# Kernel tuning notes

Hardware: AMD Instinct MI355X
Metric: run time of the kernel (lower is better)

## Reference

```python
import jax, jax.numpy as jnp
import numpy as np

VOCAB = 62
HID = 100
NLAYERS = 3
B, T = 512, 1024


def setup_inputs() -> dict:
    key = jax.random.key(0)
    ks = jax.random.split(key, 8)
    s = 1.0 / np.sqrt(HID)  # PyTorch RNN init scale
    input_ids = jax.random.randint(ks[0], (B, T), 0, VOCAB, dtype=jnp.int32)
    emb = jax.random.normal(ks[1], (VOCAB, HID), dtype=jnp.float32)
    W_ih = jax.random.uniform(ks[2], (NLAYERS, HID, HID), jnp.float32, -s, s)
    W_hh = jax.random.uniform(ks[3], (NLAYERS, HID, HID), jnp.float32, -s, s)
    b_ih = jax.random.uniform(ks[4], (NLAYERS, HID), jnp.float32, -s, s)
    b_hh = jax.random.uniform(ks[5], (NLAYERS, HID), jnp.float32, -s, s)
    W_dec = jax.random.uniform(ks[6], (VOCAB, HID), jnp.float32, -s, s)
    b_dec = jax.random.uniform(ks[7], (VOCAB,), jnp.float32, -s, s)
    return {
        "input_ids": input_ids,
        "emb": emb,
        "W_ih": W_ih,
        "W_hh": W_hh,
        "b_ih": b_ih,
        "b_hh": b_hh,
        "W_dec": W_dec,
        "b_dec": b_dec,
    }


def _rnn_forward(x, W_ih, W_hh, b_ih, b_hh):
    # x: [B, T, H]; multi-layer tanh RNN, zero initial hidden (hidden=None path)
    bsz = x.shape[0]
    finals = []
    layer_in = jnp.swapaxes(x, 0, 1)  # time-major [T, B, H]
    for l in range(NLAYERS):
        Wi, Wh = W_ih[l], W_hh[l]
        bi, bh = b_ih[l], b_hh[l]
        # precompute input projection for whole sequence (one big GEMM)
        xin = jnp.einsum("tbh,kh->tbk", layer_in, Wi) + bi + bh

        def step(h, xt):
            h_new = jnp.tanh(xt + h @ Wh.T)
            return h_new, h_new

        h0 = jnp.zeros((bsz, HID), dtype=x.dtype)
        h_final, ys = jax.lax.scan(step, h0, xin)
        finals.append(h_final)
        layer_in = ys
    out = jnp.swapaxes(layer_in, 0, 1)  # [B, T, H]
    hidden = jnp.stack(finals, axis=0)  # [NLAYERS, B, H]
    return out, hidden


def reference(input_ids, emb, W_ih, W_hh, b_ih, b_hh, W_dec, b_dec):
    x = emb[input_ids]  # [B, T, H] embedding lookup
    rnn_out, hidden = _rnn_forward(x, W_ih, W_hh, b_ih, b_hh)
    logits = jnp.einsum("bth,vh->btv", rnn_out, W_dec) + b_dec  # [B, T, VOCAB]
    return logits, hidden
```

## Files before the change

### kernel.cpp

```cpp
#include <hip/hip_runtime.h>

#define BB 512
#define TT 1024
#define HH 100
#define HP 112
#define VV 62
#define BTV (512*1024*62)

#define OFF_EP  52428800
#define OFF_WP  52435000
#define OFF_BS  52491000
#define OFF_WDT 52491200
#define OFF_BDP 52497600

__device__ inline float tanh_fast(float x){
  float ax = fabsf(x);
  float e  = __expf(2.0f*ax);
  float r  = 1.0f - __fdividef(2.0f, e + 1.0f);
  return copysignf(r, x);
}

__global__ void prep_kernel(
    const float* __restrict__ emb, const float* __restrict__ W_ih,
    const float* __restrict__ W_hh,
    const float* __restrict__ b_ih, const float* __restrict__ b_hh,
    const float* __restrict__ W_dec, const float* __restrict__ b_dec,
    float* __restrict__ ws)
{
  int g = blockIdx.x*256 + threadIdx.x;
  if (g < 6200){
    int v = g/100, k = g%100;
    float a = b_ih[k] + b_hh[k];
    const float* er = emb + v*100;
    const float* wr = W_ih + k*100;
    for (int h=0; h<100; h++) a = fmaf(er[h], wr[h], a);
    ws[OFF_EP + v*100 + k] = a;
  } else if (g < 62200){
    int i = g - 6200;
    int u = i/11200, r = i%11200;
    int k = r/112, h = r%112;
    int l = (u+1)>>1;
    const float* src = (u & 1) ? W_ih : W_hh;
    ws[OFF_WP + i] = (h < HH) ? src[l*10000 + k*100 + h] : 0.f;
  } else if (g < 62400){
    int i = g - 62200;
    int l = i/100 + 1, k = i%100;
    ws[OFF_BS + i] = b_ih[l*100+k] + b_hh[l*100+k];
  } else if (g < 68800){
    int i = g - 62400;
    int h = i/64, v = i%64;
    ws[OFF_WDT + i] = (v < VV) ? W_dec[v*100 + h] : 0.f;
  } else if (g < 68864){
    int i = g - 68800;
    ws[OFF_BDP + i] = (i < VV) ? b_dec[i] : 0.f;
  }
}

#define BARRIER() do{ asm volatile("s_waitcnt lgkmcnt(0)" ::: "memory"); \
                      __builtin_amdgcn_s_barrier(); \
                      asm volatile("" ::: "memory"); }while(0)

__global__ __launch_bounds__(512, 2) void fused_rnn(
    const int* __restrict__ ids, const float* __restrict__ ws,
    float* __restrict__ buf, float* __restrict__ hid)
{
  __shared__ float ep_s[6200];
  __shared__ int   ids_s[2][TT];
  __shared__ float hs[2][3][HP];
  __shared__ float zz[2][2][HH];

  const int tid = threadIdx.x;
  const int bA = blockIdx.x;
  const int bB = blockIdx.x + 256;

  int u = tid / 100;
  int L = tid - u*100;
  const bool act = (tid < 500);
  if (!act){ u = 4; L = 99; }
  const int o4 = (L & ~3);
  const int sq = L & 3;
  const bool is_b0 = (L & 1);
  const bool is_b1 = (L & 2);

  float4 w[4][7];
  #pragma unroll
  for (int j=0;j<4;j++){
    const float4* wr = (const float4*)(ws + OFF_WP + u*11200 + (o4+j)*HP + 28*sq);
    #pragma unroll
    for (int i=0;i<7;i++) w[j][i] = wr[i];
  }
  float binit[4] = {0.f,0.f,0.f,0.f};
  if ((u==1 || u==3) && sq==0){
    const float* bsrow = ws + OFF_BS + (u==3 ? 100 : 0);
    #pragma unroll
    for (int j=0;j<4;j++) binit[j] = bsrow[o4+j];
  }

  for (int i=tid;i<6200;i+=512) ep_s[i] = ws[OFF_EP+i];
  for (int i=tid;i<TT;i+=512){
    ids_s[0][i] = ids[(size_t)bA*TT + i];
    ids_s[1][i] = ids[(size_t)bB*TT + i];
  }
  for (int i=tid;i<2*3*HP;i+=512) ((float*)hs)[i] = 0.f;
  __syncthreads();

  const int lin = (u<=1) ? 0 : (u<=3 ? 1 : 2);
  const float* hinA = &hs[0][lin][28*sq];
  const float* hinB = &hs[1][lin][28*sq];

  int idnA = ids_s[0][1], idnB = ids_s[1][1];
  float epxA = ep_s[ids_s[0][0]*HH + L];
  float epxB = ep_s[ids_s[1][0]*HH + L];
  float epxA_n = 0.f, epxB_n = 0.f;

  float* stA = buf + (size_t)bA*HH + L;
  float* stB = buf + (size_t)bB*HH + L;

  auto quad_reduce = [&](float a0,float a1,float a2,float a3)->float{
    float sA = is_b0 ? a0 : a1, kA = is_b0 ? a1 : a0;
    float A  = kA + __shfl_xor(sA, 1);
    float sB = is_b0 ? a2 : a3, kB = is_b0 ? a3 : a2;
    float Bq = kB + __shfl_xor(sB, 1);
    float sC = is_b1 ? A : Bq, kC = is_b1 ? Bq : A;
    return kC + __shfl_xor(sC, 2);
  };

  for (int s=0; s<TT+2; ++s){
    float aA0=binit[0], aA1=binit[1], aA2=binit[2], aA3=binit[3];
    float aB0=binit[0], aB1=binit[1], aB2=binit[2], aB3=binit[3];
    #pragma unroll
    for (int i=0;i<7;i++){
      float4 ha = ((const float4*)hinA)[i];
      float4 hb = ((const float4*)hinB)[i];
      float4 w0=w[0][i], w1=w[1][i], w2=w[2][i], w3=w[3][i];
      aA0=fmaf(ha.x,w0.x,aA0); aA0=fmaf(ha.y,w0.y,aA0); aA0=fmaf(ha.z,w0.z,aA0); aA0=fmaf(ha.w,w0.w,aA0);
      aA1=fmaf(ha.x,w1.x,aA1); aA1=fmaf(ha.y,w1.y,aA1); aA1=fmaf(ha.z,w1.z,aA1); aA1=fmaf(ha.w,w1.w,aA1);
      aA2=fmaf(ha.x,w2.x,aA2); aA2=fmaf(ha.y,w2.y,aA2); aA2=fmaf(ha.z,w2.z,aA2); aA2=fmaf(ha.w,w2.w,aA2);
      aA3=fmaf(ha.x,w3.x,aA3); aA3=fmaf(ha.y,w3.y,aA3); aA3=fmaf(ha.z,w3.z,aA3); aA3=fmaf(ha.w,w3.w,aA3);
      aB0=fmaf(hb.x,w0.x,aB0); aB0=fmaf(hb.y,w0.y,aB0); aB0=fmaf(hb.z,w0.z,aB0); aB0=fmaf(hb.w,w0.w,aB0);
      aB1=fmaf(hb.x,w1.x,aB1); aB1=fmaf(hb.y,w1.y,aB1); aB1=fmaf(hb.z,w1.z,aB1); aB1=fmaf(hb.w,w1.w,aB1);
      aB2=fmaf(hb.x,w2.x,aB2); aB2=fmaf(hb.y,w2.y,aB2); aB2=fmaf(hb.z,w2.z,aB2); aB2=fmaf(hb.w,w2.w,aB2);
      aB3=fmaf(hb.x,w3.x,aB3); aB3=fmaf(hb.y,w3.y,aB3); aB3=fmaf(hb.z,w3.z,aB3); aB3=fmaf(hb.w,w3.w,aB3);
    }
    float zA = quad_reduce(aA0,aA1,aA2,aA3);
    float zB = quad_reduce(aB0,aB1,aB2,aB3);

    if (u==0){
      epxA_n = ep_s[idnA*HH + L];
      epxB_n = ep_s[idnB*HH + L];
      int nid = (s+2 < TT) ? s+2 : TT-1;
      idnA = ids_s[0][nid]; idnB = ids_s[1][nid];
    }
    if (u==2){        zz[0][0][L] = zA; zz[1][0][L] = zB; }
    if (u==4 && act){ zz[0][1][L] = zA; zz[1][1][L] = zB; }
    BARRIER();

    if (u==0 && s < TT){
      float hA = tanh_fast(epxA + zA);
      float hB = tanh_fast(epxB + zB);
      hs[0][0][L] = hA; hs[1][0][L] = hB;
      epxA = epxA_n; epxB = epxB_n;
    }
    if (u==1 && (unsigned)(s-1) < TT){
      hs[0][1][L] = tanh_fast(zA + zz[0][0][L]);
      hs[1][1][L] = tanh_fast(zB + zz[1][0][L]);
    }
    if (u==3 && s >= 2){
      float hA = tanh_fast(zA + zz[0][1][L]);
      float hB = tanh_fast(zB + zz[1][1][L]);
      hs[0][2][L] = hA; hs[1][2][L] = hB;
      *stA = hA; *stB = hB;
      stA += BB*HH; stB += BB*HH;
    }
    BARRIER();
  }
  __syncthreads();

  if (tid < 300){
    int l = tid/100, k = tid - l*100;
    hid[((size_t)l*BB + bA)*HH + k] = hs[0][l][k];
    hid[((size_t)l*BB + bB)*HH + k] = hs[1][l][k];
  }
}

__global__ __launch_bounds__(128) void dec_kernel(
    const float* __restrict__ buf, const float* __restrict__ wdt,
    const float* __restrict__ bdp, float* __restrict__ out)
{
  __shared__ float rt[100*129];
  const int tid = threadIdx.x;
  const int wg  = blockIdx.x;
  const int bb  = wg >> 3;
  const int t0  = (wg & 7) * 128;
  const float4* b4 = (const float4*)buf;

  #pragma unroll
  for (int j=0;j<25;j++){
    int f = j*128 + tid;
    int i = f/25, c = f%25;
    float4 v = b4[((size_t)(t0+i)*BB + bb)*25 + c];
    rt[(4*c+0)*129 + i] = v.x;
    rt[(4*c+1)*129 + i] = v.y;
    rt[(4*c+2)*129 + i] = v.z;
    rt[(4*c+3)*129 + i] = v.w;
  }
  __syncthreads();

  float4 acc[16];
  const float4* bd4 = (const float4*)bdp;
  #pragma unroll
  for (int j=0;j<16;j++) acc[j] = bd4[j];

  for (int h=0; h<HH; h++){
    float rv = rt[h*129 + tid];
    const float4* w4 = (const float4*)(wdt + h*64);
    #pragma unroll
    for (int j=0;j<16;j++){
      float4 w = w4[j];
      acc[j].x = fmaf(rv,w.x,acc[j].x);
      acc[j].y = fmaf(rv,w.y,acc[j].y);
      acc[j].z = fmaf(rv,w.z,acc[j].z);
      acc[j].w = fmaf(rv,w.w,acc[j].w);
    }
  }

  float2* o2 = (float2*)(out + (size_t)(wg*128 + tid)*VV);
  #pragma unroll
  for (int j=0;j<15;j++){
    o2[2*j]   = make_float2(acc[j].x, acc[j].y);
    o2[2*j+1] = make_float2(acc[j].z, acc[j].w);
  }
  o2[30] = make_float2(acc[15].x, acc[15].y);
}

extern "C" void kernel_launch(void* const* d_in, const int* in_sizes, int n_in,
                              void* d_out, int out_size, void* d_ws, size_t ws_size,
                              hipStream_t stream)
{
  const int*   ids   = (const int*)d_in[0];
  const float* emb   = (const float*)d_in[1];
  const float* W_ih  = (const float*)d_in[2];
  const float* W_hh  = (const float*)d_in[3];
  const float* b_ih  = (const float*)d_in[4];
  const float* b_hh  = (const float*)d_in[5];
  const float* W_dec = (const float*)d_in[6];
  const float* b_dec = (const float*)d_in[7];
  float* out = (float*)d_out;
  float* ws  = (float*)d_ws;
  float* buf = ws;
  float* hid = out + BTV;

  prep_kernel<<<269, 256, 0, stream>>>(emb, W_ih, W_hh, b_ih, b_hh, W_dec, b_dec, ws);
  fused_rnn <<<256, 512, 0, stream>>>(ids, ws, buf, hid);
  dec_kernel<<<4096, 128, 0, stream>>>(buf, ws+OFF_WDT, ws+OFF_BDP, out);
}
```

Before: 1.518 ms.

## Restructure fused RNN to one barrier per step with double-buffered hidden state

Reassigns the hidden-state work so each layer's input and recurrent matvecs for one output row are done by the same lane group. This removes the intermediate zz exchange and halves the barriers per timestep, using double-buffered hidden-state tiles in shared memory. It also uses packed v2f FMAs and DPP cross-lane reductions instead of shuffles, writes the intermediate buffer batch-major so the decoder reads contiguous rows, and writes final hidden states inline. In exchange each lane holds 112 weight floats in registers, which adds register pressure under launch_bounds(512,2).

Result: faster. 1.369 ms (-9.8%).

```diff
diff --git a/kernel.cpp b/kernel.cpp
--- a/kernel.cpp
+++ b/kernel.cpp
@@ -3,21 +3,29 @@
 #define BB 512
 #define TT 1024
 #define HH 100
-#define HP 112
 #define VV 62
 #define BTV (512*1024*62)
 
 #define OFF_EP  52428800
-#define OFF_WP  52435000
-#define OFF_BS  52491000
-#define OFF_WDT 52491200
-#define OFF_BDP 52497600
+#define OFF_WU  52435200
+#define OFF_BS  52491200
+#define OFF_WDT 52491400
+#define OFF_BDP 52497800
+
+typedef float v2f __attribute__((ext_vector_type(2)));
 
 __device__ inline float tanh_fast(float x){
   float ax = fabsf(x);
   float e  = __expf(2.0f*ax);
   float r  = 1.0f - __fdividef(2.0f, e + 1.0f);
   return copysignf(r, x);
+}
+
+__device__ inline float dpp_xor1(float x){
+  return __int_as_float(__builtin_amdgcn_update_dpp(0, __float_as_int(x), 0xB1, 0xF, 0xF, true));
+}
+__device__ inline float dpp_xor2(float x){
+  return __int_as_float(__builtin_amdgcn_update_dpp(0, __float_as_int(x), 0x4E, 0xF, 0xF, true));
 }
 
 __global__ void prep_kernel(
@@ -37,11 +45,30 @@
     ws[OFF_EP + v*100 + k] = a;
   } else if (g < 62200){
     int i = g - 6200;
-    int u = i/11200, r = i%11200;
-    int k = r/112, h = r%112;
-    int l = (u+1)>>1;
-    const float* src = (u & 1) ? W_ih : W_hh;
-    ws[OFF_WP + i] = (h < HH) ? src[l*10000 + k*100 + h] : 0.f;
+    int u, base;
+    if (i < 11200){ u=0; base=i; }
+    else if (i < 33600){ u=1; base=i-11200; }
+    else { u=2; base=i-33600; }
+    int lane = base/112, e = base%112;
+    int j = e/56, c = e%56;
+    float val;
+    if (u==0){
+      int q = lane&1, rp = lane>>1;
+      int r = rp + 50*j;
+      int col = 56*q + c;
+      val = (col < HH) ? W_hh[r*HH + col] : 0.f;
+    } else {
+      int q = lane&3, rp = lane>>2;
+      int r = rp + 50*j;
+      if (q < 2){
+        int col = 56*q + c;
+        val = (col < HH) ? W_ih[u*10000 + r*HH + col] : 0.f;
+      } else {
+        int col = 56*(q-2) + c;
+        val = (col < HH) ? W_hh[u*10000 + r*HH + col] : 0.f;
+      }
+    }
+    ws[OFF_WU + i] = val;
   } else if (g < 62400){
     int i = g - 62200;
     int l = i/100 + 1, k = i%100;
@@ -56,44 +83,42 @@
   }
 }
 
-#define BARRIER() do{ asm volatile("s_waitcnt lgkmcnt(0)" ::: "memory"); \
-                      __builtin_amdgcn_s_barrier(); \
-                      asm volatile("" ::: "memory"); }while(0)
-
 __global__ __launch_bounds__(512, 2) void fused_rnn(
     const int* __restrict__ ids, const float* __restrict__ ws,
     float* __restrict__ buf, float* __restrict__ hid)
 {
   __shared__ float ep_s[6200];
   __shared__ int   ids_s[2][TT];
-  __shared__ float hs[2][3][HP];
-  __shared__ float zz[2][2][HH];
+  __shared__ float hs[2][2][3][112];
 
   const int tid = threadIdx.x;
-  const int bA = blockIdx.x;
-  const int bB = blockIdx.x + 256;
-
-  int u = tid / 100;
-  int L = tid - u*100;
-  const bool act = (tid < 500);
-  if (!act){ u = 4; L = 99; }
-  const int o4 = (L & ~3);
-  const int sq = L & 3;
-  const bool is_b0 = (L & 1);
-  const bool is_b1 = (L & 2);
-
-  float4 w[4][7];
-  #pragma unroll
-  for (int j=0;j<4;j++){
-    const float4* wr = (const float4*)(ws + OFF_WP + u*11200 + (o4+j)*HP + 28*sq);
+  const int bA = blockIdx.x, bB = blockIdx.x + 256;
+
+  int u, l; bool act = true;
+  if (tid < 100){ u=0; l=tid; }
+  else if (tid < 300){ u=1; l=tid-100; }
+  else if (tid < 500){ u=2; l=tid-300; }
+  else { u=2; l=199; act=false; }
+
+  int q, rp, lv, col0;
+  if (u==0){ q = l&1; rp = l>>1; lv = 0; col0 = 56*q; }
+  else     { q = l&3; rp = l>>2; lv = (u==1) ? ((q<2)?0:1) : ((q<2)?1:2); col0 = 56*(q&1); }
+
+  v2f w[56];
+  {
+    int ubase = (u==0) ? 0 : (u==1) ? 11200 : 33600;
+    const float4* ws4 = (const float4*)(ws + OFF_WU + ubase + l*112);
     #pragma unroll
-    for (int i=0;i<7;i++) w[j][i] = wr[i];
-  }
-  float binit[4] = {0.f,0.f,0.f,0.f};
-  if ((u==1 || u==3) && sq==0){
-    const float* bsrow = ws + OFF_BS + (u==3 ? 100 : 0);
-    #pragma unroll
-    for (int j=0;j<4;j++) binit[j] = bsrow[o4+j];
+    for (int i=0;i<28;i++){
+      float4 t = ws4[i];
+      w[2*i]   = (v2f){t.x, t.y};
+      w[2*i+1] = (v2f){t.z, t.w};
+    }
+  }
+  float bias0 = 0.f, bias1 = 0.f;
+  if (u != 0 && q == 0){
+    const float* bs = ws + OFF_BS + (u-1)*100;
+    bias0 = bs[rp]; bias1 = bs[rp+50];
   }
 
   for (int i=tid;i<6200;i+=512) ep_s[i] = ws[OFF_EP+i];
@@ -101,85 +126,91 @@
     ids_s[0][i] = ids[(size_t)bA*TT + i];
     ids_s[1][i] = ids[(size_t)bB*TT + i];
   }
-  for (int i=tid;i<2*3*HP;i+=512) ((float*)hs)[i] = 0.f;
+  for (int i=tid;i<2*2*3*112;i+=512) ((float*)hs)[i] = 0.f;
   __syncthreads();
 
-  const int lin = (u<=1) ? 0 : (u<=3 ? 1 : 2);
-  const float* hinA = &hs[0][lin][28*sq];
-  const float* hinB = &hs[1][lin][28*sq];
-
-  int idnA = ids_s[0][1], idnB = ids_s[1][1];
-  float epxA = ep_s[ids_s[0][0]*HH + L];
-  float epxB = ep_s[ids_s[1][0]*HH + L];
-  float epxA_n = 0.f, epxB_n = 0.f;
-
-  float* stA = buf + (size_t)bA*HH + L;
-  float* stB = buf + (size_t)bB*HH + L;
-
-  auto quad_reduce = [&](float a0,float a1,float a2,float a3)->float{
-    float sA = is_b0 ? a0 : a1, kA = is_b0 ? a1 : a0;
-    float A  = kA + __shfl_xor(sA, 1);
-    float sB = is_b0 ? a2 : a3, kB = is_b0 ? a3 : a2;
-    float Bq = kB + __shfl_xor(sB, 1);
-    float sC = is_b1 ? A : Bq, kC = is_b1 ? Bq : A;
-    return kC + __shfl_xor(sC, 2);
-  };
-
-  for (int s=0; s<TT+2; ++s){
-    float aA0=binit[0], aA1=binit[1], aA2=binit[2], aA3=binit[3];
-    float aB0=binit[0], aB1=binit[1], aB2=binit[2], aB3=binit[3];
+  const float4* h4 = (const float4*)hs;
+  const int c4 = col0 >> 2;
+  const int iA = (0*3 + lv)*28 + c4;
+  const int iB = (1*3 + lv)*28 + c4;
+  float* hw = (float*)hs;
+
+  int idn = 0; float epx0 = 0.f, epx1 = 0.f;
+  if (u == 0){
+    int id0 = ids_s[q][0];
+    epx0 = ep_s[id0*HH + rp];
+    epx1 = ep_s[id0*HH + rp+50];
+    idn  = ids_s[q][1];
+  }
+  const int X  = q >> 1;
+  const int rr = rp + 50*(q & 1);
+  float* stp = buf + ((size_t)(X ? bB : bA))*TT*HH + rr;
+
+  for (int s = 0; s < TT + 2; ++s){
+    const int po = (s & 1) ? 0 : 168;
+    const int wo = (s & 1) ? 672 : 0;
+
+    v2f aA0 = {bias0, 0.f}, aA1 = {bias1, 0.f};
+    v2f aB0 = {bias0, 0.f}, aB1 = {bias1, 0.f};
     #pragma unroll
-    for (int i=0;i<7;i++){
-      float4 ha = ((const float4*)hinA)[i];
-      float4 hb = ((const float4*)hinB)[i];
-      float4 w0=w[0][i], w1=w[1][i], w2=w[2][i], w3=w[3][i];
-      aA0=fmaf(ha.x,w0.x,aA0); aA0=fmaf(ha.y,w0.y,aA0); aA0=fmaf(ha.z,w0.z,aA0); aA0=fmaf(ha.w,w0.w,aA0);
-      aA1=fmaf(ha.x,w1.x,aA1); aA1=fmaf(ha.y,w1.y,aA1); aA1=fmaf(ha.z,w1.z,aA1); aA1=fmaf(ha.w,w1.w,aA1);
-      aA2=fmaf(ha.x,w2.x,aA2); aA2=fmaf(ha.y,w2.y,aA2); aA2=fmaf(ha.z,w2.z,aA2); aA2=fmaf(ha.w,w2.w,aA2);
-      aA3=fmaf(ha.x,w3.x,aA3); aA3=fmaf(ha.y,w3.y,aA3); aA3=fmaf(ha.z,w3.z,aA3); aA3=fmaf(ha.w,w3.w,aA3);
-      aB0=fmaf(hb.x,w0.x,aB0); aB0=fmaf(hb.y,w0.y,aB0); aB0=fmaf(hb.z,w0.z,aB0); aB0=fmaf(hb.w,w0.w,aB0);
-      aB1=fmaf(hb.x,w1.x,aB1); aB1=fmaf(hb.y,w1.y,aB1); aB1=fmaf(hb.z,w1.z,aB1); aB1=fmaf(hb.w,w1.w,aB1);
-      aB2=fmaf(hb.x,w2.x,aB2); aB2=fmaf(hb.y,w2.y,aB2); aB2=fmaf(hb.z,w2.z,aB2); aB2=fmaf(hb.w,w2.w,aB2);
-      aB3=fmaf(hb.x,w3.x,aB3); aB3=fmaf(hb.y,w3.y,aB3); aB3=fmaf(hb.z,w3.z,aB3); aB3=fmaf(hb.w,w3.w,aB3);
-    }
-    float zA = quad_reduce(aA0,aA1,aA2,aA3);
-    float zB = quad_reduce(aB0,aB1,aB2,aB3);
-
-    if (u==0){
-      epxA_n = ep_s[idnA*HH + L];
-      epxB_n = ep_s[idnB*HH + L];
-      int nid = (s+2 < TT) ? s+2 : TT-1;
-      idnA = ids_s[0][nid]; idnB = ids_s[1][nid];
-    }
-    if (u==2){        zz[0][0][L] = zA; zz[1][0][L] = zB; }
-    if (u==4 && act){ zz[0][1][L] = zA; zz[1][1][L] = zB; }
-    BARRIER();
-
-    if (u==0 && s < TT){
-      float hA = tanh_fast(epxA + zA);
-      float hB = tanh_fast(epxB + zB);
-      hs[0][0][L] = hA; hs[1][0][L] = hB;
-      epxA = epxA_n; epxB = epxB_n;
-    }
-    if (u==1 && (unsigned)(s-1) < TT){
-      hs[0][1][L] = tanh_fast(zA + zz[0][0][L]);
-      hs[1][1][L] = tanh_fast(zB + zz[1][0][L]);
-    }
-    if (u==3 && s >= 2){
-      float hA = tanh_fast(zA + zz[0][1][L]);
-      float hB = tanh_fast(zB + zz[1][1][L]);
-      hs[0][2][L] = hA; hs[1][2][L] = hB;
-      *stA = hA; *stB = hB;
-      stA += BB*HH; stB += BB*HH;
-    }
-    BARRIER();
-  }
-  __syncthreads();
-
-  if (tid < 300){
-    int l = tid/100, k = tid - l*100;
-    hid[((size_t)l*BB + bA)*HH + k] = hs[0][l][k];
-    hid[((size_t)l*BB + bB)*HH + k] = hs[1][l][k];
+    for (int i=0;i<14;i++){
+      float4 ha = h4[iA + po + i];
+      float4 hb = h4[iB + po + i];
+      v2f h0 = {ha.x, ha.y}, h1 = {ha.z, ha.w};
+      v2f g0 = {hb.x, hb.y}, g1 = {hb.z, hb.w};
+      aA0 = __builtin_elementwise_fma(w[2*i],    h0, aA0);
+      aA0 = __builtin_elementwise_fma(w[2*i+1],  h1, aA0);
+      aA1 = __builtin_elementwise_fma(w[28+2*i], h0, aA1);
+      aA1 = __builtin_elementwise_fma(w[29+2*i], h1, aA1);
+      aB0 = __builtin_elementwise_fma(w[2*i],    g0, aB0);
+      aB0 = __builtin_elementwise_fma(w[2*i+1],  g1, aB0);
+      aB1 = __builtin_elementwise_fma(w[28+2*i], g0, aB1);
+      aB1 = __builtin_elementwise_fma(w[29+2*i], g1, aB1);
+    }
+    float zA0 = aA0.x + aA0.y;
+    float zA1 = aA1.x + aA1.y;
+    float zB0 = aB0.x + aB0.y;
+    float zB1 = aB1.x + aB1.y;
+    zA0 += dpp_xor1(zA0); zA1 += dpp_xor1(zA1);
+    zB0 += dpp_xor1(zB0); zB1 += dpp_xor1(zB1);
+    if (u){
+      zA0 += dpp_xor2(zA0); zA1 += dpp_xor2(zA1);
+      zB0 += dpp_xor2(zB0); zB1 += dpp_xor2(zB1);
+    }
+
+    if (u == 0){
+      if (s < TT){
+        float za = q ? zB0 : zA0;
+        float zb = q ? zB1 : zA1;
+        float h0v = tanh_fast(epx0 + za);
+        float h1v = tanh_fast(epx1 + zb);
+        hw[wo + (q*3 + 0)*112 + rp]      = h0v;
+        hw[wo + (q*3 + 0)*112 + rp + 50] = h1v;
+        if (s == TT-1){
+          int bX = q ? bB : bA;
+          hid[(size_t)bX*HH + rp]      = h0v;
+          hid[(size_t)bX*HH + rp + 50] = h1v;
+        }
+        epx0 = ep_s[idn*HH + rp];
+        epx1 = ep_s[idn*HH + rp + 50];
+        idn  = ids_s[q][(s+2 < TT) ? s+2 : TT-1];
+      }
+    } else {
+      float zs = (q & 1) ? (X ? zB1 : zA1) : (X ? zB0 : zA0);
+      bool on = (u == 1) ? ((unsigned)(s-1) < TT) : (s >= 2);
+      if (on & act){
+        float hv = tanh_fast(zs);
+        hw[wo + (X*3 + u)*112 + rr] = hv;
+        if (u == 2){ *stp = hv; stp += HH; }
+        int bX = X ? bB : bA;
+        if (u == 1 && s == TT)     hid[((size_t)BB   + bX)*HH + rr] = hv;
+        if (u == 2 && s == TT+1)   hid[((size_t)2*BB + bX)*HH + rr] = hv;
+      }
+    }
+
+    asm volatile("s_waitcnt lgkmcnt(0)" ::: "memory");
+    __builtin_amdgcn_s_barrier();
+    asm volatile("" ::: "memory");
   }
 }
 
@@ -193,12 +224,13 @@
   const int bb  = wg >> 3;
   const int t0  = (wg & 7) * 128;
   const float4* b4 = (const float4*)buf;
+  const size_t rb = ((size_t)bb*TT + t0)*25;
 
   #pragma unroll
   for (int j=0;j<25;j++){
     int f = j*128 + tid;
     int i = f/25, c = f%25;
-    float4 v = b4[((size_t)(t0+i)*BB + bb)*25 + c];
+    float4 v = b4[rb + f];
     rt[(4*c+0)*129 + i] = v.x;
     rt[(4*c+1)*129 + i] = v.y;
     rt[(4*c+2)*129 + i] = v.z;
@@ -224,7 +256,7 @@
     }
   }
 
-  float2* o2 = (float2*)(out + (size_t)(wg*128 + tid)*VV);
+  float2* o2 = (float2*)(out + ((size_t)bb*TT + t0 + tid)*VV);
   #pragma unroll
   for (int j=0;j<15;j++){
     o2[2*j]   = make_float2(acc[j].x, acc[j].y);
```
